# Optimization experiments

Hardware: AMD Instinct MI355X
Metric: run time of the kernel (lower is better)

Reference implementation:

```python
import jax, jax.numpy as jnp
import numpy as np

N, D, H, E = 4096, 512, 8, 131072
HD = D // H


def _ln(x, g, b):
    mu = x.mean(-1, keepdims=True)
    v = ((x - mu) ** 2).mean(-1, keepdims=True)
    return (x - mu) / jnp.sqrt(v + 1e-5) * g + b


def setup_inputs() -> dict:
    key = jax.random.key(0)
    ks = jax.random.split(key, 12)
    p = lambda k, s: jax.random.normal(k, s, jnp.float32) * 0.02
    return {
        "x": jax.random.normal(ks[0], (N, D), jnp.float32),
        "edge_index": jax.random.randint(ks[1], (2, E), 0, N, dtype=jnp.int32),
        "ln1_g": jnp.ones((D,), jnp.float32), "ln1_b": jnp.zeros((D,), jnp.float32),
        "ln2_g": jnp.ones((D,), jnp.float32), "ln2_b": jnp.zeros((D,), jnp.float32),
        "ln3_g": jnp.ones((D,), jnp.float32), "ln3_b": jnp.zeros((D,), jnp.float32),
        "in_proj_w": p(ks[2], (3 * D, D)), "in_proj_b": jnp.zeros((3 * D,), jnp.float32),
        "out_proj_w": p(ks[3], (D, D)), "out_proj_b": jnp.zeros((D,), jnp.float32),
        "msg_w": p(ks[4], (D, 2 * D)), "msg_b": jnp.zeros((D,), jnp.float32),
        "gru_wih": p(ks[5], (3 * D, D)), "gru_whh": p(ks[6], (3 * D, D)),
        "gru_bih": jnp.zeros((3 * D,), jnp.float32), "gru_bhh": jnp.zeros((3 * D,), jnp.float32),
        "ffn_w1": p(ks[7], (4 * D, D)), "ffn_b1": jnp.zeros((4 * D,), jnp.float32),
        "ffn_w2": p(ks[8], (D, 4 * D)), "ffn_b2": jnp.zeros((D,), jnp.float32),
        "gate_w": p(ks[9], (1, 2 * D)), "gate_b": jnp.zeros((1,), jnp.float32),
    }


def reference(x, edge_index, ln1_g, ln1_b, ln2_g, ln2_b, ln3_g, ln3_b,
              in_proj_w, in_proj_b, out_proj_w, out_proj_b,
              msg_w, msg_b, gru_wih, gru_whh, gru_bih, gru_bhh,
              ffn_w1, ffn_b1, ffn_w2, ffn_b2, gate_w, gate_b):
    src, dst = edge_index[0], edge_index[1]
    # --- MPNN branch: gather-concat-linear-scatter + GRU update ---
    xn1 = _ln(x, ln1_g, ln1_b)
    msgs = jnp.concatenate([xn1[src], xn1[dst]], axis=-1) @ msg_w.T + msg_b  # [E, D]
    aggr = jnp.zeros_like(xn1).at[dst].add(msgs)                              # scatter-add
    deg = jnp.zeros((N,), x.dtype).at[dst].add(1.0)
    aggr = aggr / jnp.clip(deg, 1.0)[:, None]
    # torch GRUCell(input=aggr, hidden=xn1)
    gi = aggr @ gru_wih.T + gru_bih
    gh = xn1 @ gru_whh.T + gru_bhh
    ir, iz, inn = jnp.split(gi, 3, axis=-1)
    hr, hz, hn = jnp.split(gh, 3, axis=-1)
    r = jax.nn.sigmoid(ir + hr)
    z = jax.nn.sigmoid(iz + hz)
    n = jnp.tanh(inn + r * hn)
    x_mpnn = (1.0 - z) * n + z * xn1
    # --- global multi-head attention over all nodes (batch of 1) ---
    xn2 = _ln(x, ln2_g, ln2_b)
    qkv = xn2 @ in_proj_w.T + in_proj_b
    q, k, v = jnp.split(qkv, 3, axis=-1)
    q = q.reshape(N, H, HD)
    k = k.reshape(N, H, HD)
    v = v.reshape(N, H, HD)
    scores = jnp.einsum('nhd,mhd->hnm', q, k) / np.float32(np.sqrt(HD))  # [H, N, N]
    w = jax.nn.softmax(scores, axis=-1)
    ctx = jnp.einsum('hnm,mhd->nhd', w, v).reshape(N, D)
    x_attn = ctx @ out_proj_w.T + out_proj_b
    attn_weights = w.mean(axis=0)[None]  # torch averages heads -> [1, N, N]
    # --- gated combine + residual ---
    g = jax.nn.sigmoid(jnp.concatenate([x_mpnn, x_attn], axis=-1) @ gate_w.T + gate_b)
    xc = x + g * x_mpnn + (1.0 - g) * x_attn
    # --- FFN (exact GELU, as torch nn.GELU default) ---
    h = jax.nn.gelu(_ln(xc, ln3_g, ln3_b) @ ffn_w1.T + ffn_b1, approximate=False)
    out = xc + (h @ ffn_w2.T + ffn_b2)
    return out, attn_weights
```

## Files before the change

### kernel.cpp

```cpp
#include <hip/hip_runtime.h>
#include <stdint.h>

#define N_ 4096
#define D_ 512
#define H_ 8
#define E_ 131072
#define TD_ 1536
#define FD_ 2048
#define CM_ 2048

typedef unsigned short u16;
typedef __bf16 bf16x8 __attribute__((ext_vector_type(8)));
typedef u16 u16x8 __attribute__((ext_vector_type(8)));
typedef u16 u16x4 __attribute__((ext_vector_type(4)));
typedef float f32x4 __attribute__((ext_vector_type(4)));

__device__ __forceinline__ u16 f2bf(float f) {
  union { float f; uint32_t u; } v; v.f = f;
  return (u16)((v.u + 0x7FFFu + ((v.u >> 16) & 1u)) >> 16);
}
__device__ __forceinline__ float bf2f(u16 b) {
  union { uint32_t u; float f; } v; v.u = ((uint32_t)b) << 16; return v.f;
}

__device__ __forceinline__ void gload16(const u16* g, u16* l) {
  __builtin_amdgcn_global_load_lds(
      (const __attribute__((address_space(1))) void*)(uintptr_t)g,
      (__attribute__((address_space(3))) void*)(uint32_t)(uintptr_t)l, 16, 0, 0);
}

template <int BM, int BN, int BK, int WM, int WN, int FM, int FN, int MODE, bool BIAS,
          int HM, int AMODE>
__global__ __launch_bounds__(WM * WN * 64) void gemm_bt(
    const u16* __restrict__ A, int lda, const u16* __restrict__ B, int ldb,
    void* __restrict__ Cout, int ldc, const float* __restrict__ bias,
    float scale, int Kchunk, size_t hA, size_t hB, size_t hC,
    float* __restrict__ rowm, const float* __restrict__ rowinv,
    const int* __restrict__ auxI)
{
  static_assert(BM == WM * FM * 16 && BN == WN * FN * 16, "tile shape");
  static_assert(BK == 64, "LDS swizzle assumes BK=64");
  __shared__ alignas(16) u16 As[BM * BK];
  __shared__ alignas(16) u16 Bs[BN * BK];
  __shared__ float rsum[2][BM];
  constexpr int NT = WM * WN * 64;
  const int tid = threadIdx.x;
  const int lane = tid & 63;
  const int wave = tid >> 6;
  const long tm = (long)blockIdx.x * BM;
  long tn, k0;
  size_t cOff = 0;
  int hIdx = 0;
  if constexpr (HM == 1) {
    hIdx = blockIdx.z;
    A += (size_t)blockIdx.z * hA; B += (size_t)blockIdx.z * hB; cOff = (size_t)blockIdx.z * hC;
    tn = (long)blockIdx.y * BN; k0 = 0;
  } else if constexpr (HM == 2) {
    hIdx = blockIdx.y;
    A += (size_t)blockIdx.y * hA; B += (size_t)blockIdx.y * hB; cOff = (size_t)blockIdx.y * hC;
    tn = 0; k0 = (long)blockIdx.z * Kchunk;
  } else {
    tn = (long)blockIdx.y * BN; k0 = (long)blockIdx.z * Kchunk;
  }
  const int wm0 = (wave / WN) * (FM * 16);
  const int wn0 = (wave % WN) * (FN * 16);

  f32x4 acc[FM][FN] = {};

  constexpr int A_LOADS = (BM * BK) / (NT * 8);
  constexpr int B_LOADS = (BN * BK) / (NT * 8);

  for (int kt = 0; kt < Kchunk; kt += BK) {
    const long kb = k0 + kt;
#pragma unroll
    for (int i = 0; i < A_LOADS; ++i) {
      if constexpr (AMODE == 0) {
        int sB = (i * NT + wave * 64) * 8;
        int s = sB + lane * 8;
        int row = s / BK;
        int blk = (s % BK) >> 3;
        gload16(A + (tm + row) * (long)lda + kb + ((blk ^ (row & 7)) << 3), As + sB);
      } else {
        int s = (i * NT + tid) * 8;
        int row = s / BK, kk = s % BK;
        const float* Af = (const float*)A;
        f32x4 lo = *(const f32x4*)(Af + (tm + row) * (long)lda + kb + kk);
        f32x4 hi = *(const f32x4*)(Af + (tm + row) * (long)lda + kb + kk + 4);
        u16x8 w;
#pragma unroll
        for (int k = 0; k < 4; ++k) { w[k] = f2bf(lo[k]); w[4 + k] = f2bf(hi[k]); }
        *(u16x8*)(&As[row * BK + (kk ^ ((row & 7) << 3))]) = w;
      }
    }
#pragma unroll
    for (int i = 0; i < B_LOADS; ++i) {
      int sB = (i * NT + wave * 64) * 8;
      int s = sB + lane * 8;
      int row = s / BK;
      int blk = (s % BK) >> 3;
      gload16(B + (tn + row) * (long)ldb + kb + ((blk ^ (row & 7)) << 3), Bs + sB);
    }
    __syncthreads();
#pragma unroll
    for (int kk = 0; kk < BK; kk += 32) {
      bf16x8 af[FM], bfr[FN];
#pragma unroll
      for (int i = 0; i < FM; ++i) {
        int ar = wm0 + i * 16 + (lane & 15);
        int ac = kk + (lane >> 4) * 8;
        af[i] = *(const bf16x8*)(&As[ar * BK + (ac ^ ((ar & 7) << 3))]);
      }
#pragma unroll
      for (int j = 0; j < FN; ++j) {
        int br = wn0 + j * 16 + (lane & 15);
        int bc = kk + (lane >> 4) * 8;
        bfr[j] = *(const bf16x8*)(&Bs[br * BK + (bc ^ ((br & 7) << 3))]);
      }
#pragma unroll
      for (int i = 0; i < FM; ++i)
#pragma unroll
        for (int j = 0; j < FN; ++j)
          acc[i][j] = __builtin_amdgcn_mfma_f32_16x16x32_bf16(af[i], bfr[j], acc[i][j], 0, 0, 0);
    }
    __syncthreads();
  }

  if constexpr (MODE == 5) {
#pragma unroll
    for (int i = 0; i < FM; ++i) {
      float part[4] = {0.0f, 0.0f, 0.0f, 0.0f};
#pragma unroll
      for (int j = 0; j < FN; ++j) {
        const long col = tn + wn0 + j * 16 + (lane & 15);
#pragma unroll
        for (int r = 0; r < 4; ++r) {
          const long row = tm + wm0 + i * 16 + (lane >> 4) * 4 + r;
          float p = expf(acc[i][j][r] * scale);
          ((u16*)Cout)[cOff + row * (long)ldc + col] = f2bf(p);
          part[r] += p;
        }
      }
#pragma unroll
      for (int r = 0; r < 4; ++r) {
        float s = part[r];
        s += __shfl_xor(s, 1); s += __shfl_xor(s, 2);
        s += __shfl_xor(s, 4); s += __shfl_xor(s, 8);
        if ((lane & 15) == 0)
          rsum[wave & 1][wm0 + i * 16 + (lane >> 4) * 4 + r] = s;
      }
    }
    __syncthreads();
    for (int t = tid; t < BM; t += NT)
      atomicAdd(&rowm[(size_t)hIdx * CM_ + tm + t], rsum[0][t] + rsum[1][t]);
    return;
  }

#pragma unroll
  for (int i = 0; i < FM; ++i) {
#pragma unroll
    for (int j = 0; j < FN; ++j) {
      const long col = tn + wn0 + j * 16 + (lane & 15);
      float bv = 0.0f;
      if constexpr (BIAS) {
        if (MODE != 2 || blockIdx.z == 0) bv = bias[col];
      }
#pragma unroll
      for (int r = 0; r < 4; ++r) {
        const long row = tm + wm0 + i * 16 + (lane >> 4) * 4 + r;
        float v = acc[i][j][r] * scale + bv;
        if constexpr (MODE == 0) {
          ((float*)Cout)[cOff + row * (long)ldc + col] = v;
        } else if constexpr (MODE == 1) {
          ((u16*)Cout)[cOff + row * (long)ldc + col] = f2bf(v);
        } else if constexpr (MODE == 2) {
          atomicAdd(&((float*)Cout)[cOff + row * (long)ldc + col], v);
        } else if constexpr (MODE == 3) {
          float ge = 0.5f * v * (1.0f + erff(v * 0.70710678118654752f));
          ((u16*)Cout)[cOff + row * (long)ldc + col] = f2bf(ge);
        } else if constexpr (MODE == 4) {
          ((float*)Cout)[cOff + row * (long)ldc + col] = v + rowm[row * (long)ldc + col];
        } else if constexpr (MODE == 6) {
          float inv = 1.0f / rowm[(size_t)hIdx * CM_ + row];
          atomicAdd(&((float*)Cout)[cOff + row * (long)ldc + col], v * inv);
        } else {
          float dg = (float)auxI[row];
          float p2 = rowm[(size_t)row * 2048 + 1536 + col];
          float vv = (v + dg * (p2 + rowinv[col])) / fmaxf(dg, 1.0f);
          ((u16*)Cout)[cOff + row * (long)ldc + col] = f2bf(vv);
        }
      }
    }
  }
}


__global__ void conv_weights(const float* __restrict__ ip, const float* __restrict__ wih,
    const float* __restrict__ whh, const float* __restrict__ op,
    const float* __restrict__ f1, const float* __restrict__ f2, const float* __restrict__ mw,
    const float* __restrict__ gbhh,
    u16* __restrict__ ipb, u16* __restrict__ wihb, u16* __restrict__ whhb,
    u16* __restrict__ opb, u16* __restrict__ f1b, u16* __restrict__ f2b,
    u16* __restrict__ w1b, u16* __restrict__ w2b, float* __restrict__ biascat)
{
  int i = (blockIdx.x * 256 + threadIdx.x) * 4;
  if (i >= 5244928) return;
  if (i >= 5242880) {
    int j = i - 5242880;
#pragma unroll
    for (int k = 0; k < 4; ++k) biascat[j + k] = (j + k < TD_) ? gbhh[j + k] : 0.0f;
    return;
  }
  if (i >= 4718592) {
    int j = i - 4718592;
    int r = j >> 10, c = j & 1023;
    f32x4 v = *(const f32x4*)(mw + j);
    u16* d = (c < 512 ? w1b + r * 512 + c : w2b + r * 512 + (c - 512));
#pragma unroll
    for (int k = 0; k < 4; ++k) d[k] = f2bf(v[k]);
    return;
  }
  const float* src; u16* dst; int off;
  if      (i < 786432)  { src = ip;  dst = ipb;  off = i; }
  else if (i < 1572864) { src = wih; dst = wihb; off = i - 786432; }
  else if (i < 2359296) { src = whh; dst = whhb; off = i - 1572864; }
  else if (i < 2621440) { src = op;  dst = opb;  off = i - 2359296; }
  else if (i < 3670016) { src = f1;  dst = f1b;  off = i - 2621440; }
  else                  { src = f2;  dst = f2b;  off = i - 3670016; }
  f32x4 v = *(const f32x4*)(src + off);
#pragma unroll
  for (int k = 0; k < 4; ++k) dst[off + k] = f2bf(v[k]);
}

__global__ __launch_bounds__(1024) void transpose_bf16(const u16* __restrict__ src, int sld,
                                                       u16* __restrict__ dst, int dld) {
  __shared__ u16 tile[32][33];
  int r = blockIdx.y * 32 + threadIdx.y;
  int c = blockIdx.x * 32 + threadIdx.x;
  tile[threadIdx.y][threadIdx.x] = src[(size_t)r * sld + c];
  __syncthreads();
  int rr = blockIdx.x * 32 + threadIdx.y;
  int cc = blockIdx.y * 32 + threadIdx.x;
  dst[(size_t)rr * dld + cc] = tile[threadIdx.x][threadIdx.y];
}

__global__ void hist_kernel(const int* __restrict__ ei, int* __restrict__ degi) {
  int e = blockIdx.x * 256 + threadIdx.x;
  atomicAdd(&degi[ei[E_ + e]], 1);
}

__global__ __launch_bounds__(1024) void scan_kernel(const int* __restrict__ degi,
    int* __restrict__ rowstart, int* __restrict__ cursor) {
  __shared__ int sums[1024];
  int t = threadIdx.x;
  int b = t * 4;
  int d0 = degi[b], d1 = degi[b + 1], d2 = degi[b + 2], d3 = degi[b + 3];
  int tot = d0 + d1 + d2 + d3;
  sums[t] = tot;
  __syncthreads();
  for (int off = 1; off < 1024; off <<= 1) {
    int v = (t >= off) ? sums[t - off] : 0;
    __syncthreads();
    sums[t] += v;
    __syncthreads();
  }
  int excl = (t > 0) ? sums[t - 1] : 0;
  rowstart[b] = excl; rowstart[b + 1] = excl + d0;
  rowstart[b + 2] = excl + d0 + d1; rowstart[b + 3] = excl + d0 + d1 + d2;
  cursor[b] = excl; cursor[b + 1] = excl + d0;
  cursor[b + 2] = excl + d0 + d1; cursor[b + 3] = excl + d0 + d1 + d2;
  if (t == 1023) rowstart[N_] = excl + tot;
}

__global__ void scatter_kernel(const int* __restrict__ ei, int* __restrict__ cursor,
                               int* __restrict__ ss) {
  int e = blockIdx.x * 256 + threadIdx.x;
  int d = ei[E_ + e];
  int pos = atomicAdd(&cursor[d], 1);
  ss[pos] = ei[e];
}

__global__ __launch_bounds__(128) void gather_kernel(const int* __restrict__ rs,
    const int* __restrict__ ss, const u16* __restrict__ xn1b, u16* __restrict__ gsb) {
  int dst = blockIdx.x, t = threadIdx.x;
  int s0 = rs[dst], s1 = rs[dst + 1];
  __shared__ int sl[128];
  float a0 = 0, a1 = 0, a2 = 0, a3 = 0;
  for (int base = s0; base < s1; base += 128) {
    int n = min(128, s1 - base);
    if (t < n) sl[t] = ss[base + t];
    __syncthreads();
    for (int j = 0; j < n; ++j) {
      u16x4 v = *(const u16x4*)(xn1b + (size_t)sl[j] * D_ + t * 4);
      a0 += bf2f(v[0]); a1 += bf2f(v[1]); a2 += bf2f(v[2]); a3 += bf2f(v[3]);
    }
    __syncthreads();
  }
  u16* dp = gsb + (size_t)dst * D_ + t * 4;
  dp[0] = f2bf(a0); dp[1] = f2bf(a1); dp[2] = f2bf(a2); dp[3] = f2bf(a3);
}

__global__ __launch_bounds__(128) void ln12_kernel(const float* __restrict__ x,
    const float* __restrict__ g1, const float* __restrict__ b1,
    const float* __restrict__ g2, const float* __restrict__ b2,
    u16* __restrict__ xn1b, u16* __restrict__ xn2b)
{
  int row = blockIdx.x, t = threadIdx.x;
  size_t base = (size_t)row * D_ + t * 4;
  f32x4 v = *(const f32x4*)(x + base);
  float s = v[0] + v[1] + v[2] + v[3];
  float ss = v[0]*v[0] + v[1]*v[1] + v[2]*v[2] + v[3]*v[3];
  __shared__ float red[4];
  for (int off = 32; off; off >>= 1) { s += __shfl_down(s, off); ss += __shfl_down(ss, off); }
  if ((t & 63) == 0) { red[t >> 6] = s; red[2 + (t >> 6)] = ss; }
  __syncthreads();
  s = red[0] + red[1]; ss = red[2] + red[3];
  float mu = s * (1.0f / D_);
  float inv = rsqrtf(ss * (1.0f / D_) - mu * mu + 1e-5f);
#pragma unroll
  for (int i = 0; i < 4; ++i) {
    int c = t * 4 + i;
    float xh = (v[i] - mu) * inv;
    xn1b[base + i] = f2bf(xh * g1[c] + b1[c]);
    xn2b[base + i] = f2bf(xh * g2[c] + b2[c]);
  }
}

__global__ void gru_kernel(const float* __restrict__ gi, const float* __restrict__ ghp,
                           const u16* __restrict__ xn1b, float* __restrict__ xm) {
  int i = blockIdx.x * 256 + threadIdx.x;
  int n = i >> 9, d = i & 511;
  size_t bi = (size_t)n * TD_ + d;
  size_t bh = (size_t)n * 2048 + d;
  float ir = gi[bi], iz = gi[bi + 512], in_ = gi[bi + 1024];
  float hr = ghp[bh], hz = ghp[bh + 512], hn = ghp[bh + 1024];
  float r = 1.0f / (1.0f + expf(-(ir + hr)));
  float z = 1.0f / (1.0f + expf(-(iz + hz)));
  float nn = tanhf(in_ + r * hn);
  xm[i] = (1.0f - z) * nn + z * bf2f(xn1b[i]);
}

__global__ __launch_bounds__(256) void mean_kernel(const u16* __restrict__ sc,
    const float* __restrict__ rowsum, float* __restrict__ attn) {
  const int row = blockIdx.x, t = threadIdx.x;
  float am[16] = {};
  for (int h = 0; h < H_; ++h) {
    const u16* wr = sc + (size_t)h * ((size_t)CM_ * N_) + (size_t)row * N_ + t * 16;
    float inv = 0.125f / rowsum[(size_t)h * CM_ + row];
    u16x8 v0 = *(const u16x8*)(wr);
    u16x8 v1 = *(const u16x8*)(wr + 8);
#pragma unroll
    for (int i = 0; i < 8; ++i) { am[i] += bf2f(v0[i]) * inv; am[8 + i] += bf2f(v1[i]) * inv; }
  }
  float* ar = attn + (size_t)row * N_ + t * 16;
#pragma unroll
  for (int i = 0; i < 16; ++i) ar[i] = am[i];
}

__global__ __launch_bounds__(128) void combine_ln3(const float* __restrict__ x,
    const float* __restrict__ xm, const float* __restrict__ xa,
    const float* __restrict__ gw, const float* __restrict__ gb,
    const float* __restrict__ g3, const float* __restrict__ b3,
    float* __restrict__ xc, u16* __restrict__ xn3b)
{
  int row = blockIdx.x, t = threadIdx.x;
  size_t base = (size_t)row * D_ + t * 4;
  f32x4 xv = *(const f32x4*)(x + base);
  f32x4 mv = *(const f32x4*)(xm + base);
  f32x4 av = *(const f32x4*)(xa + base);
  __shared__ float red[4];
  float gs = 0.0f;
#pragma unroll
  for (int i = 0; i < 4; ++i) { int c = t * 4 + i; gs += mv[i] * gw[c] + av[i] * gw[D_ + c]; }
  for (int off = 32; off; off >>= 1) gs += __shfl_down(gs, off);
  if ((t & 63) == 0) red[t >> 6] = gs;
  __syncthreads();
  float g = 1.0f / (1.0f + expf(-(red[0] + red[1] + gb[0])));
  __syncthreads();
  f32x4 cv = xv + g * mv + (1.0f - g) * av;
  *(f32x4*)(xc + base) = cv;
  float s = cv[0] + cv[1] + cv[2] + cv[3];
  float ss = cv[0]*cv[0] + cv[1]*cv[1] + cv[2]*cv[2] + cv[3]*cv[3];
  for (int off = 32; off; off >>= 1) { s += __shfl_down(s, off); ss += __shfl_down(ss, off); }
  if ((t & 63) == 0) { red[t >> 6] = s; red[2 + (t >> 6)] = ss; }
  __syncthreads();
  s = red[0] + red[1]; ss = red[2] + red[3];
  float mu = s * (1.0f / D_);
  float inv = rsqrtf(ss * (1.0f / D_) - mu * mu + 1e-5f);
#pragma unroll
  for (int i = 0; i < 4; ++i) {
    int c = t * 4 + i;
    float xh = (cv[i] - mu) * inv;
    xn3b[base + i] = f2bf(xh * g3[c] + b3[c]);
  }
}


extern "C" void kernel_launch(void* const* d_in, const int* in_sizes, int n_in,
                              void* d_out, int out_size, void* d_ws, size_t ws_size,
                              hipStream_t stream)
{
  (void)in_sizes; (void)n_in; (void)out_size;
  const float* x         = (const float*)d_in[0];
  const int*   ei        = (const int*)d_in[1];
  const float* ln1_g     = (const float*)d_in[2];
  const float* ln1_b     = (const float*)d_in[3];
  const float* ln2_g     = (const float*)d_in[4];
  const float* ln2_b     = (const float*)d_in[5];
  const float* ln3_g     = (const float*)d_in[6];
  const float* ln3_b     = (const float*)d_in[7];
  const float* in_proj_w = (const float*)d_in[8];
  const float* in_proj_b = (const float*)d_in[9];
  const float* out_proj_w= (const float*)d_in[10];
  const float* out_proj_b= (const float*)d_in[11];
  const float* msg_w     = (const float*)d_in[12];
  const float* msg_b     = (const float*)d_in[13];
  const float* gru_wih   = (const float*)d_in[14];
  const float* gru_whh   = (const float*)d_in[15];
  const float* gru_bih   = (const float*)d_in[16];
  const float* gru_bhh   = (const float*)d_in[17];
  const float* ffn_w1    = (const float*)d_in[18];
  const float* ffn_b1    = (const float*)d_in[19];
  const float* ffn_w2    = (const float*)d_in[20];
  const float* ffn_b2    = (const float*)d_in[21];
  const float* gate_w    = (const float*)d_in[22];
  const float* gate_b    = (const float*)d_in[23];

  char* ws = (char*)d_ws;
  size_t o = 0;
  auto alloc = [&](size_t b) { size_t r = o; o += (b + 255) & ~(size_t)255; return r; };
  const size_t o_xn1b  = alloc((size_t)N_ * D_ * 2);
  const size_t o_xn2b  = alloc((size_t)N_ * D_ * 2);
  const size_t o_ipb   = alloc((size_t)TD_ * D_ * 2);
  const size_t o_w1b   = alloc((size_t)D_ * D_ * 2);
  const size_t o_wihb  = alloc((size_t)TD_ * D_ * 2);
  const size_t o_whhb  = alloc((size_t)TD_ * D_ * 2);
  const size_t o_w2b   = alloc((size_t)D_ * D_ * 2);
  const size_t o_opb   = alloc((size_t)D_ * D_ * 2);
  const size_t o_f1b   = alloc((size_t)FD_ * D_ * 2);
  const size_t o_f2b   = alloc((size_t)D_ * FD_ * 2);
  const size_t o_bcat  = alloc((size_t)2048 * 4);
  const size_t o_degi  = alloc((size_t)N_ * 4);
  const size_t o_rs    = alloc((size_t)(N_ + 1) * 4);
  const size_t o_cur   = alloc((size_t)N_ * 4);
  const size_t o_ss    = alloc((size_t)E_ * 4);
  const size_t o_rsum  = alloc((size_t)H_ * N_ * 4);
  const size_t o_aggrb = alloc((size_t)N_ * D_ * 2);
  const size_t o_gsb   = alloc((size_t)N_ * D_ * 2);
  const size_t o_xm    = alloc((size_t)N_ * D_ * 4);
  const size_t o_xn3b  = alloc((size_t)N_ * D_ * 2);
  const size_t o_big1  = alloc((size_t)H_ * CM_ * N_ * 2);
  const size_t o_big2  = alloc((size_t)N_ * FD_ * 2);
  const size_t o_rn    = alloc((size_t)N_ * TD_ * 4);
  const size_t o_ro    = alloc((size_t)N_ * 2048 * 4);
  if (ws_size < o) return;

  u16* xn1b   = (u16*)(ws + o_xn1b);
  u16* xn2b   = (u16*)(ws + o_xn2b);
  u16* ipb    = (u16*)(ws + o_ipb);
  u16* w1b    = (u16*)(ws + o_w1b);
  u16* wihb   = (u16*)(ws + o_wihb);
  u16* whhb   = (u16*)(ws + o_whhb);
  u16* w2b    = (u16*)(ws + o_w2b);
  u16* opb    = (u16*)(ws + o_opb);
  u16* f1b    = (u16*)(ws + o_f1b);
  u16* f2b    = (u16*)(ws + o_f2b);
  float* bcat = (float*)(ws + o_bcat);
  int* degi   = (int*)(ws + o_degi);
  int* rs     = (int*)(ws + o_rs);
  int* cur    = (int*)(ws + o_cur);
  int* ssrc   = (int*)(ws + o_ss);
  float* rsumA= (float*)(ws + o_rsum);
  u16* aggrb  = (u16*)(ws + o_aggrb);
  u16* gsb    = (u16*)(ws + o_gsb);
  float* xm   = (float*)(ws + o_xm);
  u16* xn3b   = (u16*)(ws + o_xn3b);
  u16* scc    = (u16*)(ws + o_big1);
  u16* h1b    = (u16*)(ws + o_big2);
  float* gi   = (float*)(ws + o_rn);
  u16* qkvb   = (u16*)(ws + o_rn);
  u16* vT     = (u16*)(ws + o_rn + (size_t)N_ * TD_ * 2);
  float* ctx  = (float*)(ws + o_rn + (size_t)N_ * TD_ * 2 + (size_t)D_ * N_ * 2);
  float* ghp  = (float*)(ws + o_ro);
  float* xattn= (float*)(ws + o_ro);
  float* xc   = (float*)(ws + o_ro + (size_t)N_ * D_ * 4);

  float* outp = (float*)d_out;
  float* attn = (float*)d_out + (size_t)N_ * D_;

  hipMemsetAsync(degi, 0, (size_t)N_ * 4, stream);
  hipMemsetAsync(rsumA, 0, (size_t)H_ * N_ * 4, stream);

  conv_weights<<<5122, 256, 0, stream>>>(in_proj_w, gru_wih, gru_whh, out_proj_w,
                                         ffn_w1, ffn_w2, msg_w, gru_bhh,
                                         ipb, wihb, whhb, opb, f1b, f2b, w1b, w2b, bcat);

  ln12_kernel<<<N_, 128, 0, stream>>>(x, ln1_g, ln1_b, ln2_g, ln2_b, xn1b, xn2b);

  hist_kernel<<<512, 256, 0, stream>>>(ei, degi);
  scan_kernel<<<1, 1024, 0, stream>>>(degi, rs, cur);
  scatter_kernel<<<512, 256, 0, stream>>>(ei, cur, ssrc);
  gather_kernel<<<N_, 128, 0, stream>>>(rs, ssrc, xn1b, gsb);

  gemm_bt<128, 128, 64, 2, 2, 4, 4, 0, true, 0, 0><<<dim3(32, 16), 256, 0, stream>>>(
      xn1b, D_, whhb, D_, ghp, 2048, bcat, 1.0f, D_, 0, 0, 0, nullptr, nullptr, nullptr);
  gemm_bt<64, 64, 64, 2, 2, 2, 2, 7, false, 0, 0><<<dim3(64, 8), 256, 0, stream>>>(
      gsb, D_, w1b, D_, aggrb, D_, nullptr, 1.0f, D_, 0, 0, 0, ghp, msg_b, degi);

  gemm_bt<128, 128, 64, 2, 2, 4, 4, 0, true, 0, 0><<<dim3(32, 12), 256, 0, stream>>>(
      aggrb, D_, wihb, D_, gi, TD_, gru_bih, 1.0f, D_, 0, 0, 0, nullptr, nullptr, nullptr);
  gru_kernel<<<8192, 256, 0, stream>>>(gi, ghp, xn1b, xm);

  gemm_bt<128, 128, 64, 2, 2, 4, 4, 1, true, 0, 0><<<dim3(32, 12), 256, 0, stream>>>(
      xn2b, D_, ipb, D_, qkvb, TD_, in_proj_b, 1.0f, D_, 0, 0, 0, nullptr, nullptr, nullptr);
  transpose_bf16<<<dim3(16, 128), dim3(32, 32), 0, stream>>>(qkvb + 1024, TD_, vT, N_);
  hipMemsetAsync(ctx, 0, (size_t)N_ * D_ * 4, stream);

  for (int c = 0; c < N_ / CM_; ++c) {
    float* rsumC = rsumA + (size_t)c * H_ * CM_;
    gemm_bt<128, 128, 64, 2, 2, 4, 4, 5, false, 1, 0><<<dim3(CM_ / 128, 32, 8), 256, 0, stream>>>(
        qkvb + (size_t)c * CM_ * TD_, TD_, qkvb + 512, TD_, scc, N_, nullptr,
        0.125f, 64, 64, 64, (size_t)CM_ * N_, rsumC, nullptr, nullptr);
    mean_kernel<<<CM_, 256, 0, stream>>>(scc, rsumC, attn + (size_t)c * CM_ * N_);
    gemm_bt<64, 64, 64, 2, 2, 2, 2, 6, false, 2, 0><<<dim3(CM_ / 64, 8, 8), 256, 0, stream>>>(
        scc, N_, vT, N_, ctx + (size_t)c * CM_ * D_, D_, nullptr, 1.0f, 512,
        (size_t)CM_ * N_, (size_t)64 * N_, 64, rsumC, nullptr, nullptr);
  }

  gemm_bt<64, 64, 64, 2, 2, 2, 2, 0, true, 0, 2><<<dim3(64, 8), 256, 0, stream>>>(
      (const u16*)ctx, D_, opb, D_, xattn, D_, out_proj_b, 1.0f, D_, 0, 0, 0,
      nullptr, nullptr, nullptr);

  combine_ln3<<<N_, 128, 0, stream>>>(x, xm, xattn, gate_w, gate_b, ln3_g, ln3_b, xc, xn3b);

  gemm_bt<128, 128, 64, 2, 2, 4, 4, 3, true, 0, 0><<<dim3(32, 16), 256, 0, stream>>>(
      xn3b, D_, f1b, D_, h1b, FD_, ffn_b1, 1.0f, D_, 0, 0, 0, nullptr, nullptr, nullptr);
  gemm_bt<64, 64, 64, 2, 2, 2, 2, 4, true, 0, 0><<<dim3(64, 8), 256, 0, stream>>>(
      h1b, FD_, f2b, FD_, outp, D_, ffn_b2, 1.0f, FD_, 0, 0, 0, xc, nullptr, nullptr);
}
```

Measured before the change: 572.7 us.

## Fuse attention into rowsum pass plus fused softmax-PV-headmean kernel

Replaces the chunked QK^T GEMM, materialized bf16 score buffer, mean kernel and PV GEMM with two kernels. A first pass recomputes QK^T to accumulate softmax row sums. A second pass recomputes scores, normalizes them, accumulates the head-averaged attention weights in registers, stages probabilities in LDS and multiplies them by V with atomic adds into ctx. This removes the large 8xN×N intermediate write/read in exchange for computing QK^T twice and loading Q/K directly from global memory without LDS tiling.

```diff
diff --git a/kernel.cpp b/kernel.cpp
--- a/kernel.cpp
+++ b/kernel.cpp
@@ -7,7 +7,6 @@
 #define E_ 131072
 #define TD_ 1536
 #define FD_ 2048
-#define CM_ 2048
 
 typedef unsigned short u16;
 typedef __bf16 bf16x8 __attribute__((ext_vector_type(8)));
@@ -29,39 +28,30 @@
       (__attribute__((address_space(3))) void*)(uint32_t)(uintptr_t)l, 16, 0, 0);
 }
 
+__device__ __forceinline__ f32x4 mfma16(bf16x8 a, bf16x8 b, f32x4 c) {
+  return __builtin_amdgcn_mfma_f32_16x16x32_bf16(a, b, c, 0, 0, 0);
+}
+
 template <int BM, int BN, int BK, int WM, int WN, int FM, int FN, int MODE, bool BIAS,
-          int HM, int AMODE>
+          int AMODE>
 __global__ __launch_bounds__(WM * WN * 64) void gemm_bt(
     const u16* __restrict__ A, int lda, const u16* __restrict__ B, int ldb,
     void* __restrict__ Cout, int ldc, const float* __restrict__ bias,
-    float scale, int Kchunk, size_t hA, size_t hB, size_t hC,
-    float* __restrict__ rowm, const float* __restrict__ rowinv,
+    float scale, int Kchunk,
+    const float* __restrict__ rowm, const float* __restrict__ rowinv,
     const int* __restrict__ auxI)
 {
   static_assert(BM == WM * FM * 16 && BN == WN * FN * 16, "tile shape");
   static_assert(BK == 64, "LDS swizzle assumes BK=64");
   __shared__ alignas(16) u16 As[BM * BK];
   __shared__ alignas(16) u16 Bs[BN * BK];
-  __shared__ float rsum[2][BM];
   constexpr int NT = WM * WN * 64;
   const int tid = threadIdx.x;
   const int lane = tid & 63;
   const int wave = tid >> 6;
   const long tm = (long)blockIdx.x * BM;
-  long tn, k0;
-  size_t cOff = 0;
-  int hIdx = 0;
-  if constexpr (HM == 1) {
-    hIdx = blockIdx.z;
-    A += (size_t)blockIdx.z * hA; B += (size_t)blockIdx.z * hB; cOff = (size_t)blockIdx.z * hC;
-    tn = (long)blockIdx.y * BN; k0 = 0;
-  } else if constexpr (HM == 2) {
-    hIdx = blockIdx.y;
-    A += (size_t)blockIdx.y * hA; B += (size_t)blockIdx.y * hB; cOff = (size_t)blockIdx.y * hC;
-    tn = 0; k0 = (long)blockIdx.z * Kchunk;
-  } else {
-    tn = (long)blockIdx.y * BN; k0 = (long)blockIdx.z * Kchunk;
-  }
+  const long tn = (long)blockIdx.y * BN;
+  const long k0 = (long)blockIdx.z * Kchunk;
   const int wm0 = (wave / WN) * (FM * 16);
   const int wn0 = (wave % WN) * (FN * 16);
 
@@ -120,39 +110,9 @@
       for (int i = 0; i < FM; ++i)
 #pragma unroll
         for (int j = 0; j < FN; ++j)
-          acc[i][j] = __builtin_amdgcn_mfma_f32_16x16x32_bf16(af[i], bfr[j], acc[i][j], 0, 0, 0);
-    }
-    __syncthreads();
-  }
-
-  if constexpr (MODE == 5) {
-#pragma unroll
-    for (int i = 0; i < FM; ++i) {
-      float part[4] = {0.0f, 0.0f, 0.0f, 0.0f};
-#pragma unroll
-      for (int j = 0; j < FN; ++j) {
-        const long col = tn + wn0 + j * 16 + (lane & 15);
-#pragma unroll
-        for (int r = 0; r < 4; ++r) {
-          const long row = tm + wm0 + i * 16 + (lane >> 4) * 4 + r;
-          float p = expf(acc[i][j][r] * scale);
-          ((u16*)Cout)[cOff + row * (long)ldc + col] = f2bf(p);
-          part[r] += p;
-        }
-      }
-#pragma unroll
-      for (int r = 0; r < 4; ++r) {
-        float s = part[r];
-        s += __shfl_xor(s, 1); s += __shfl_xor(s, 2);
-        s += __shfl_xor(s, 4); s += __shfl_xor(s, 8);
-        if ((lane & 15) == 0)
-          rsum[wave & 1][wm0 + i * 16 + (lane >> 4) * 4 + r] = s;
-      }
-    }
-    __syncthreads();
-    for (int t = tid; t < BM; t += NT)
-      atomicAdd(&rowm[(size_t)hIdx * CM_ + tm + t], rsum[0][t] + rsum[1][t]);
-    return;
+          acc[i][j] = mfma16(af[i], bfr[j], acc[i][j]);
+    }
+    __syncthreads();
   }
 
 #pragma unroll
@@ -160,37 +120,175 @@
 #pragma unroll
     for (int j = 0; j < FN; ++j) {
       const long col = tn + wn0 + j * 16 + (lane & 15);
-      float bv = 0.0f;
-      if constexpr (BIAS) {
-        if (MODE != 2 || blockIdx.z == 0) bv = bias[col];
-      }
+      float bv = BIAS ? bias[col] : 0.0f;
 #pragma unroll
       for (int r = 0; r < 4; ++r) {
         const long row = tm + wm0 + i * 16 + (lane >> 4) * 4 + r;
         float v = acc[i][j][r] * scale + bv;
         if constexpr (MODE == 0) {
-          ((float*)Cout)[cOff + row * (long)ldc + col] = v;
+          ((float*)Cout)[row * (long)ldc + col] = v;
         } else if constexpr (MODE == 1) {
-          ((u16*)Cout)[cOff + row * (long)ldc + col] = f2bf(v);
-        } else if constexpr (MODE == 2) {
-          atomicAdd(&((float*)Cout)[cOff + row * (long)ldc + col], v);
+          ((u16*)Cout)[row * (long)ldc + col] = f2bf(v);
         } else if constexpr (MODE == 3) {
           float ge = 0.5f * v * (1.0f + erff(v * 0.70710678118654752f));
-          ((u16*)Cout)[cOff + row * (long)ldc + col] = f2bf(ge);
+          ((u16*)Cout)[row * (long)ldc + col] = f2bf(ge);
         } else if constexpr (MODE == 4) {
-          ((float*)Cout)[cOff + row * (long)ldc + col] = v + rowm[row * (long)ldc + col];
-        } else if constexpr (MODE == 6) {
-          float inv = 1.0f / rowm[(size_t)hIdx * CM_ + row];
-          atomicAdd(&((float*)Cout)[cOff + row * (long)ldc + col], v * inv);
+          ((float*)Cout)[row * (long)ldc + col] = v + rowm[row * (long)ldc + col];
         } else {
           float dg = (float)auxI[row];
           float p2 = rowm[(size_t)row * 2048 + 1536 + col];
           float vv = (v + dg * (p2 + rowinv[col])) / fmaxf(dg, 1.0f);
-          ((u16*)Cout)[cOff + row * (long)ldc + col] = f2bf(vv);
+          ((u16*)Cout)[row * (long)ldc + col] = f2bf(vv);
         }
       }
     }
   }
+}
+
+
+__global__ __launch_bounds__(256) void attn_rowsum(
+    const u16* __restrict__ qkvb, float* __restrict__ rowsum)
+{
+  const int tid = threadIdx.x;
+  const int lane = tid & 63;
+  const int w = tid >> 6;
+  const int q0 = blockIdx.x * 32;
+  const int h = blockIdx.y;
+  const int c = lane & 15, g = lane >> 4;
+  bf16x8 aQ[2][2];
+#pragma unroll
+  for (int ti = 0; ti < 2; ++ti)
+#pragma unroll
+    for (int f = 0; f < 2; ++f)
+      aQ[ti][f] = *(const bf16x8*)(qkvb + (size_t)(q0 + ti * 16 + c) * TD_ +
+                                   h * 64 + f * 32 + g * 8);
+  float part[2][4] = {};
+  for (int kt = w * 128; kt < N_; kt += 512) {
+#pragma unroll
+    for (int kj = 0; kj < 8; ++kj) {
+      bf16x8 bK[2];
+#pragma unroll
+      for (int f = 0; f < 2; ++f)
+        bK[f] = *(const bf16x8*)(qkvb + (size_t)(kt + kj * 16 + c) * TD_ +
+                                 512 + h * 64 + f * 32 + g * 8);
+#pragma unroll
+      for (int ti = 0; ti < 2; ++ti) {
+        f32x4 s = {0.0f, 0.0f, 0.0f, 0.0f};
+        s = mfma16(aQ[ti][0], bK[0], s);
+        s = mfma16(aQ[ti][1], bK[1], s);
+#pragma unroll
+        for (int r = 0; r < 4; ++r) part[ti][r] += __expf(s[r] * 0.125f);
+      }
+    }
+  }
+#pragma unroll
+  for (int m = 1; m <= 8; m <<= 1)
+#pragma unroll
+    for (int ti = 0; ti < 2; ++ti)
+#pragma unroll
+      for (int r = 0; r < 4; ++r) part[ti][r] += __shfl_xor(part[ti][r], m);
+  if (c == 0) {
+#pragma unroll
+    for (int ti = 0; ti < 2; ++ti)
+#pragma unroll
+      for (int r = 0; r < 4; ++r)
+        atomicAdd(&rowsum[(size_t)h * N_ + q0 + ti * 16 + g * 4 + r], part[ti][r]);
+  }
+}
+
+__global__ __launch_bounds__(256) void attn_fused(
+    const u16* __restrict__ qkvb, const u16* __restrict__ vT,
+    const float* __restrict__ rowsum, float* __restrict__ ctx,
+    float* __restrict__ attn)
+{
+  __shared__ u16 P[32 * 512];
+  __shared__ float invs[H_][32];
+  const int tid = threadIdx.x;
+  const int lane = tid & 63;
+  const int w = tid >> 6;
+  const int q0 = blockIdx.x * 32;
+  const int kc0 = blockIdx.y * 512;
+  const int c = lane & 15, g = lane >> 4;
+  if (tid < H_ * 32) {
+    int hh = tid >> 5, qq = tid & 31;
+    invs[hh][qq] = 1.0f / rowsum[(size_t)hh * N_ + q0 + qq];
+  }
+  __syncthreads();
+  float att[2][8][4] = {};
+  const int tiw = w & 1;
+  const int djb = (w >> 1) * 2;
+  for (int h = 0; h < H_; ++h) {
+    bf16x8 aQ[2][2];
+#pragma unroll
+    for (int ti = 0; ti < 2; ++ti)
+#pragma unroll
+      for (int f = 0; f < 2; ++f)
+        aQ[ti][f] = *(const bf16x8*)(qkvb + (size_t)(q0 + ti * 16 + c) * TD_ +
+                                     h * 64 + f * 32 + g * 8);
+    f32x4 sacc[2][8];
+#pragma unroll
+    for (int ti = 0; ti < 2; ++ti)
+#pragma unroll
+      for (int kj = 0; kj < 8; ++kj) sacc[ti][kj] = (f32x4){0.0f, 0.0f, 0.0f, 0.0f};
+#pragma unroll
+    for (int kj = 0; kj < 8; ++kj) {
+      bf16x8 bK[2];
+#pragma unroll
+      for (int f = 0; f < 2; ++f)
+        bK[f] = *(const bf16x8*)(qkvb + (size_t)(kc0 + w * 128 + kj * 16 + c) * TD_ +
+                                 512 + h * 64 + f * 32 + g * 8);
+#pragma unroll
+      for (int ti = 0; ti < 2; ++ti) {
+        sacc[ti][kj] = mfma16(aQ[ti][0], bK[0], sacc[ti][kj]);
+        sacc[ti][kj] = mfma16(aQ[ti][1], bK[1], sacc[ti][kj]);
+      }
+    }
+#pragma unroll
+    for (int ti = 0; ti < 2; ++ti) {
+#pragma unroll
+      for (int r = 0; r < 4; ++r) {
+        const int row = ti * 16 + g * 4 + r;
+        const float iv = invs[h][row];
+#pragma unroll
+        for (int kj = 0; kj < 8; ++kj) {
+          float p = __expf(sacc[ti][kj][r] * 0.125f) * iv;
+          att[ti][kj][r] += p;
+          int col = w * 128 + kj * 16 + c;
+          P[row * 512 + (col ^ ((row & 7) << 3))] = f2bf(p);
+        }
+      }
+    }
+    __syncthreads();
+    f32x4 cacc[2] = {{0.0f, 0.0f, 0.0f, 0.0f}, {0.0f, 0.0f, 0.0f, 0.0f}};
+    const int prow = tiw * 16 + c;
+#pragma unroll
+    for (int kb = 0; kb < 16; ++kb) {
+      const int kcl = kb * 32 + g * 8;
+      bf16x8 aP = *(const bf16x8*)(&P[prow * 512 + (kcl ^ ((prow & 7) << 3))]);
+#pragma unroll
+      for (int dj = 0; dj < 2; ++dj) {
+        bf16x8 bV = *(const bf16x8*)(vT + (size_t)(h * 64 + (djb + dj) * 16 + c) * N_ +
+                                     kc0 + kcl);
+        cacc[dj] = mfma16(aP, bV, cacc[dj]);
+      }
+    }
+#pragma unroll
+    for (int dj = 0; dj < 2; ++dj)
+#pragma unroll
+      for (int r = 0; r < 4; ++r)
+        atomicAdd(&ctx[(size_t)(q0 + tiw * 16 + g * 4 + r) * D_ +
+                       h * 64 + (djb + dj) * 16 + c], cacc[dj][r]);
+    __syncthreads();
+  }
+#pragma unroll
+  for (int ti = 0; ti < 2; ++ti)
+#pragma unroll
+    for (int r = 0; r < 4; ++r) {
+      const int row = q0 + ti * 16 + g * 4 + r;
+#pragma unroll
+      for (int kj = 0; kj < 8; ++kj)
+        attn[(size_t)row * N_ + kc0 + w * 128 + kj * 16 + c] = att[ti][kj][r] * 0.125f;
+    }
 }
 
 
@@ -212,9 +310,9 @@
   }
   if (i >= 4718592) {
     int j = i - 4718592;
-    int r = j >> 10, c = j & 1023;
+    int r = j >> 10, cc = j & 1023;
     f32x4 v = *(const f32x4*)(mw + j);
-    u16* d = (c < 512 ? w1b + r * 512 + c : w2b + r * 512 + (c - 512));
+    u16* d = (cc < 512 ? w1b + r * 512 + cc : w2b + r * 512 + (cc - 512));
 #pragma unroll
     for (int k = 0; k < 4; ++k) d[k] = f2bf(v[k]);
     return;
@@ -337,23 +435,6 @@
   float z = 1.0f / (1.0f + expf(-(iz + hz)));
   float nn = tanhf(in_ + r * hn);
   xm[i] = (1.0f - z) * nn + z * bf2f(xn1b[i]);
-}
-
-__global__ __launch_bounds__(256) void mean_kernel(const u16* __restrict__ sc,
-    const float* __restrict__ rowsum, float* __restrict__ attn) {
-  const int row = blockIdx.x, t = threadIdx.x;
-  float am[16] = {};
-  for (int h = 0; h < H_; ++h) {
-    const u16* wr = sc + (size_t)h * ((size_t)CM_ * N_) + (size_t)row * N_ + t * 16;
-    float inv = 0.125f / rowsum[(size_t)h * CM_ + row];
-    u16x8 v0 = *(const u16x8*)(wr);
-    u16x8 v1 = *(const u16x8*)(wr + 8);
-#pragma unroll
-    for (int i = 0; i < 8; ++i) { am[i] += bf2f(v0[i]) * inv; am[8 + i] += bf2f(v1[i]) * inv; }
-  }
-  float* ar = attn + (size_t)row * N_ + t * 16;
-#pragma unroll
-  for (int i = 0; i < 16; ++i) ar[i] = am[i];
 }
 
 __global__ __launch_bounds__(128) void combine_ln3(const float* __restrict__ x,
@@ -448,7 +529,6 @@
   const size_t o_gsb   = alloc((size_t)N_ * D_ * 2);
   const size_t o_xm    = alloc((size_t)N_ * D_ * 4);
   const size_t o_xn3b  = alloc((size_t)N_ * D_ * 2);
-  const size_t o_big1  = alloc((size_t)H_ * CM_ * N_ * 2);
   const size_t o_big2  = alloc((size_t)N_ * FD_ * 2);
   const size_t o_rn    = alloc((size_t)N_ * TD_ * 4);
   const size_t o_ro    = alloc((size_t)N_ * 2048 * 4);
@@ -469,12 +549,11 @@
   int* rs     = (int*)(ws + o_rs);
   int* cur    = (int*)(ws + o_cur);
   int* ssrc   = (int*)(ws + o_ss);
-  float* rsumA= (float*)(ws + o_rsum);
+  float* rsum = (float*)(ws + o_rsum);
   u16* aggrb  = (u16*)(ws + o_aggrb);
   u16* gsb    = (u16*)(ws + o_gsb);
   float* xm   = (float*)(ws + o_xm);
   u16* xn3b   = (u16*)(ws + o_xn3b);
-  u16* scc    = (u16*)(ws + o_big1);
   u16* h1b    = (u16*)(ws + o_big2);
   float* gi   = (float*)(ws + o_rn);
   u16* qkvb   = (u16*)(ws + o_rn);
@@ -488,7 +567,7 @@
   float* attn = (float*)d_out + (size_t)N_ * D_;
 
   hipMemsetAsync(degi, 0, (size_t)N_ * 4, stream);
-  hipMemsetAsync(rsumA, 0, (size_t)H_ * N_ * 4, stream);
+  hipMemsetAsync(rsum, 0, (size_t)H_ * N_ * 4, stream);
 
   conv_weights<<<5122, 256, 0, stream>>>(in_proj_w, gru_wih, gru_whh, out_proj_w,
                                          ffn_w1, ffn_w2, msg_w, gru_bhh,
@@ -501,39 +580,31 @@
   scatter_kernel<<<512, 256, 0, stream>>>(ei, cur, ssrc);
   gather_kernel<<<N_, 128, 0, stream>>>(rs, ssrc, xn1b, gsb);
 
-  gemm_bt<128, 128, 64, 2, 2, 4, 4, 0, true, 0, 0><<<dim3(32, 16), 256, 0, stream>>>(
-      xn1b, D_, whhb, D_, ghp, 2048, bcat, 1.0f, D_, 0, 0, 0, nullptr, nullptr, nullptr);
-  gemm_bt<64, 64, 64, 2, 2, 2, 2, 7, false, 0, 0><<<dim3(64, 8), 256, 0, stream>>>(
-      gsb, D_, w1b, D_, aggrb, D_, nullptr, 1.0f, D_, 0, 0, 0, ghp, msg_b, degi);
-
-  gemm_bt<128, 128, 64, 2, 2, 4, 4, 0, true, 0, 0><<<dim3(32, 12), 256, 0, stream>>>(
-      aggrb, D_, wihb, D_, gi, TD_, gru_bih, 1.0f, D_, 0, 0, 0, nullptr, nullptr, nullptr);
+  gemm_bt<128, 128, 64, 2, 2, 4, 4, 0, true, 0><<<dim3(32, 16), 256, 0, stream>>>(
+      xn1b, D_, whhb, D_, ghp, 2048, bcat, 1.0f, D_, nullptr, nullptr, nullptr);
+  gemm_bt<64, 64, 64, 2, 2, 2, 2, 7, false, 0><<<dim3(64, 8), 256, 0, stream>>>(
+      gsb, D_, w1b, D_, aggrb, D_, nullptr, 1.0f, D_, ghp, msg_b, degi);
+
+  gemm_bt<128, 128, 64, 2, 2, 4, 4, 0, true, 0><<<dim3(32, 12), 256, 0, stream>>>(
+      aggrb, D_, wihb, D_, gi, TD_, gru_bih, 1.0f, D_, nullptr, nullptr, nullptr);
   gru_kernel<<<8192, 256, 0, stream>>>(gi, ghp, xn1b, xm);
 
-  gemm_bt<128, 128, 64, 2, 2, 4, 4, 1, true, 0, 0><<<dim3(32, 12), 256, 0, stream>>>(
-      xn2b, D_, ipb, D_, qkvb, TD_, in_proj_b, 1.0f, D_, 0, 0, 0, nullptr, nullptr, nullptr);
+  gemm_bt<128, 128, 64, 2, 2, 4, 4, 1, true, 0><<<dim3(32, 12), 256, 0, stream>>>(
+      xn2b, D_, ipb, D_, qkvb, TD_, in_proj_b, 1.0f, D_, nullptr, nullptr, nullptr);
   transpose_bf16<<<dim3(16, 128), dim3(32, 32), 0, stream>>>(qkvb + 1024, TD_, vT, N_);
   hipMemsetAsync(ctx, 0, (size_t)N_ * D_ * 4, stream);
 
-  for (int c = 0; c < N_ / CM_; ++c) {
-    float* rsumC = rsumA + (size_t)c * H_ * CM_;
-    gemm_bt<128, 128, 64, 2, 2, 4, 4, 5, false, 1, 0><<<dim3(CM_ / 128, 32, 8), 256, 0, stream>>>(
-        qkvb + (size_t)c * CM_ * TD_, TD_, qkvb + 512, TD_, scc, N_, nullptr,
-        0.125f, 64, 64, 64, (size_t)CM_ * N_, rsumC, nullptr, nullptr);
-    mean_kernel<<<CM_, 256, 0, stream>>>(scc, rsumC, attn + (size_t)c * CM_ * N_);
-    gemm_bt<64, 64, 64, 2, 2, 2, 2, 6, false, 2, 0><<<dim3(CM_ / 64, 8, 8), 256, 0, stream>>>(
-        scc, N_, vT, N_, ctx + (size_t)c * CM_ * D_, D_, nullptr, 1.0f, 512,
-        (size_t)CM_ * N_, (size_t)64 * N_, 64, rsumC, nullptr, nullptr);
-  }
-
-  gemm_bt<64, 64, 64, 2, 2, 2, 2, 0, true, 0, 2><<<dim3(64, 8), 256, 0, stream>>>(
-      (const u16*)ctx, D_, opb, D_, xattn, D_, out_proj_b, 1.0f, D_, 0, 0, 0,
+  attn_rowsum<<<dim3(N_ / 32, H_), 256, 0, stream>>>(qkvb, rsum);
+  attn_fused<<<dim3(N_ / 32, N_ / 512), 256, 0, stream>>>(qkvb, vT, rsum, ctx, attn);
+
+  gemm_bt<64, 64, 64, 2, 2, 2, 2, 0, true, 2><<<dim3(64, 8), 256, 0, stream>>>(
+      (const u16*)ctx, D_, opb, D_, xattn, D_, out_proj_b, 1.0f, D_,
       nullptr, nullptr, nullptr);
 
   combine_ln3<<<N_, 128, 0, stream>>>(x, xm, xattn, gate_w, gate_b, ln3_g, ln3_b, xc, xn3b);
 
-  gemm_bt<128, 128, 64, 2, 2, 4, 4, 3, true, 0, 0><<<dim3(32, 16), 256, 0, stream>>>(
-      xn3b, D_, f1b, D_, h1b, FD_, ffn_b1, 1.0f, D_, 0, 0, 0, nullptr, nullptr, nullptr);
-  gemm_bt<64, 64, 64, 2, 2, 2, 2, 4, true, 0, 0><<<dim3(64, 8), 256, 0, stream>>>(
-      h1b, FD_, f2b, FD_, outp, D_, ffn_b2, 1.0f, FD_, 0, 0, 0, xc, nullptr, nullptr);
-}
+  gemm_bt<128, 128, 64, 2, 2, 4, 4, 3, true, 0><<<dim3(32, 16), 256, 0, stream>>>(
+      xn3b, D_, f1b, D_, h1b, FD_, ffn_b1, 1.0f, D_, nullptr, nullptr, nullptr);
+  gemm_bt<64, 64, 64, 2, 2, 2, 2, 4, true, 0><<<dim3(64, 8), 256, 0, stream>>>(
+      h1b, FD_, f2b, FD_, outp, D_, ffn_b2, 1.0f, FD_, xc, nullptr, nullptr);
+}
```

Measured after the change: 790.6 us. +38.1%, slower.
